# Performance work log

Hardware: AMD Instinct MI355X
Metric: run time of the kernel (lower is better)

The kernel has to match this reference:

```python
import jax, jax.numpy as jnp
import numpy as np

B, T, U, F, H, V = 4, 512, 96, 512, 512, 256
NEG_INF = -1e30


def setup_inputs() -> dict:
    key = jax.random.key(0)
    ks = jax.random.split(key, 7)
    frames = jax.random.normal(ks[0], (B, T, F), dtype=jnp.float32)
    # guarantee num_frames >= num_labels so a valid alignment path exists
    num_frames = jax.random.randint(ks[1], (B,), T // 2, T + 1, dtype=jnp.int32)
    labels = jax.random.randint(ks[2], (B, U), 1, V + 1, dtype=jnp.int32)
    num_labels = jax.random.randint(ks[3], (B,), U // 2, U + 1, dtype=jnp.int32)
    scale = 0.02
    Wf = scale * jax.random.normal(ks[4], (F, H), dtype=jnp.float32)
    E = scale * jax.random.normal(ks[5], (V + 1, H), dtype=jnp.float32)
    Wo = scale * jax.random.normal(ks[6], (H, V + 1), dtype=jnp.float32)
    return dict(frames=frames, num_frames=num_frames, labels=labels,
                num_labels=num_labels, Wf=Wf, E=E, Wo=Wo)


def _lattice_loss(frames, num_frames, labels, num_labels, Wf, E, Wo):
    Bd, Td, _ = frames.shape
    Ud = labels.shape[1]
    # 1-gram context dependency: context state after u emitted labels is
    # 0 (start) if u == 0 else labels[u-1].  ctx: [B, U+1]
    ctx = jnp.concatenate([jnp.zeros((Bd, 1), labels.dtype), labels], axis=1)
    # locally normalized weight fn (RNN-T style joint network)
    fproj = jnp.einsum('btf,fh->bth', frames, Wf)                 # [B,T,H]
    cemb = jnp.take(E, ctx, axis=0)                               # [B,U+1,H]
    h = jnp.tanh(fproj[:, :, None, :] + cemb[:, None, :, :])      # [B,T,U+1,H]
    logits = jax.nn.log_softmax(
        jnp.einsum('btuh,hv->btuv', h, Wo), axis=-1)              # [B,T,U+1,V+1]
    blank = logits[..., 0]                                        # [B,T,U+1]
    # lexical arc weight for emitting label u+1 from state u:
    # lex[b,t,u] = logits[b,t,u, labels[b,u]]
    idx = jnp.broadcast_to(labels[:, None, :, None].astype(jnp.int32),
                           (Bd, Td, Ud, 1))
    lex = jnp.take_along_axis(logits[:, :, :Ud, :], idx, axis=3)[..., 0]  # [B,T,U]

    # forward DP under the Log semiring over the (t, u) string lattice
    alpha0 = jnp.full((Bd, Ud + 1), NEG_INF, dtype=logits.dtype).at[:, 0].set(0.0)

    def step(alpha, xs):
        blank_t, lex_t, t = xs  # [B,U+1], [B,U], scalar
        stay = alpha + blank_t
        emit = jnp.concatenate(
            [jnp.full((Bd, 1), NEG_INF, dtype=alpha.dtype),
             alpha[:, :-1] + lex_t], axis=1)
        new = jnp.logaddexp(stay, emit)
        new = jnp.where((t < num_frames)[:, None], new, alpha)
        return new, None

    xs = (jnp.swapaxes(blank, 0, 1), jnp.swapaxes(lex, 0, 1), jnp.arange(Td))
    alpha, _ = jax.lax.scan(step, alpha0, xs)
    logp = jnp.take_along_axis(alpha, num_labels[:, None].astype(jnp.int32),
                               axis=1)[:, 0]
    return -logp  # [B] negative sequence log-probability


def reference(frames, num_frames, labels, num_labels, Wf, E, Wo):
    return _lattice_loss(frames, num_frames, labels, num_labels, Wf, E, Wo)
```

## Files before the change

kernel.cpp:

```cpp
#include <hip/hip_runtime.h>
#include <hip/hip_bf16.h>


#define BB 4
#define TT 512
#define UU 96
#define FF 512
#define HH 512
#define VV 256
#define NV (VV + 1)
#define NU (UU + 1)
#define NP 272
#define NEG_INF (-1e30f)
#define LOG2E 1.4426950408889634f
#define LN2 0.6931471805599453f
#define NG 128
#define GSTRIDE 520
#define WOSCL 64.0f
#define C2SCL 0.022542110f
#define BCHUNK 17408
#define BLONGS 2176
#define SPLANE 1088

typedef _Float16 f16;
typedef __attribute__((ext_vector_type(2))) _Float16 f16x2;
typedef __attribute__((ext_vector_type(8))) _Float16 f16x8;
typedef __attribute__((ext_vector_type(2))) long longx2;
typedef __bf16 bf16;
typedef __bf16 bf16x8 __attribute__((ext_vector_type(8)));
typedef float f32x4 __attribute__((ext_vector_type(4)));

__device__ __forceinline__ f16x8 splat8(float s) {
    f16 v = (f16)s;
    f16x8 r = {v, v, v, v, v, v, v, v};
    return r;
}

__device__ __forceinline__ long tanh_pack8(f16x8 fv8, f16x8 cv8) {
    f16x8 x = fv8 + cv8;
    x = __builtin_elementwise_min(__builtin_elementwise_max(x, splat8(-2.0f)),
                                  splat8(2.0f));
    f16x8 y = x * x;
    f16x8 q = y * splat8(-0.0067528f) + splat8(0.0700672f);
    q = y * q + splat8(-0.301720f);
    q = y * q + splat8(1.0f);
    f16x8 t = x * q;
    int lo = 0, hi = 0;
    lo = __builtin_amdgcn_cvt_pk_fp8_f32((float)t[0], (float)t[1], lo, false);
    lo = __builtin_amdgcn_cvt_pk_fp8_f32((float)t[2], (float)t[3], lo, true);
    hi = __builtin_amdgcn_cvt_pk_fp8_f32((float)t[4], (float)t[5], hi, false);
    hi = __builtin_amdgcn_cvt_pk_fp8_f32((float)t[6], (float)t[7], hi, true);
    return (long)(((unsigned long long)(unsigned int)lo) |
                  (((unsigned long long)(unsigned int)hi) << 32));
}

__device__ __forceinline__ long pack_fp8x8(const float* v) {
    int lo = 0, hi = 0;
    lo = __builtin_amdgcn_cvt_pk_fp8_f32(v[0], v[1], lo, false);
    lo = __builtin_amdgcn_cvt_pk_fp8_f32(v[2], v[3], lo, true);
    hi = __builtin_amdgcn_cvt_pk_fp8_f32(v[4], v[5], hi, false);
    hi = __builtin_amdgcn_cvt_pk_fp8_f32(v[6], v[7], hi, true);
    return (long)(((unsigned long long)(unsigned int)lo) |
                  (((unsigned long long)(unsigned int)hi) << 32));
}

__device__ __forceinline__ float lae2(float x, float y) {
    float m = fmaxf(x, y);
    float d = fminf(x, y) - m;
    return m + __builtin_amdgcn_logf(1.0f + __builtin_amdgcn_exp2f(d));
}

__device__ __forceinline__ float lse3_2(float x, float y, float z) {
    float m = fmaxf(fmaxf(x, y), z);
    float s = __builtin_amdgcn_exp2f(x - m) + __builtin_amdgcn_exp2f(y - m) +
              __builtin_amdgcn_exp2f(z - m);
    return m + __builtin_amdgcn_logf(s);
}

__device__ __forceinline__ float lse5_2(float a, float b, float c, float d, float e) {
    float m = fmaxf(fmaxf(fmaxf(a, b), fmaxf(c, d)), e);
    float s = __builtin_amdgcn_exp2f(a - m) + __builtin_amdgcn_exp2f(b - m) +
              __builtin_amdgcn_exp2f(c - m) + __builtin_amdgcn_exp2f(d - m) +
              __builtin_amdgcn_exp2f(e - m);
    return m + __builtin_amdgcn_logf(s);
}

__device__ __forceinline__ void async_copy16(const void* g, void* l) {
    __builtin_amdgcn_global_load_lds(
        (const __attribute__((address_space(1))) unsigned int*)g,
        (__attribute__((address_space(3))) unsigned int*)l, 16, 0, 0);
}

__global__ __launch_bounds__(256, 2) void k_front(
    const float* __restrict__ frames, const float* __restrict__ Wf,
    const float* __restrict__ Wo, const float* __restrict__ E,
    const int* __restrict__ labels, f16* __restrict__ fproj,
    long* __restrict__ Wo_s, f16* __restrict__ cemb) {
    __shared__ bf16 Alds[64 * 40];
    __shared__ bf16 Blds[64 * 40];
    const int blk = blockIdx.x;
    const int tid = threadIdx.x;

    if (blk < 256) {
        const int r0 = (blk & 31) * 64;
        const int n0 = (blk >> 5) * 64;
        const int lane = tid & 63, w = tid >> 6;
        const int c = lane & 15, g = lane >> 4;

        const int srow = tid >> 2, sko = (tid & 3) * 8;
        const float* fptr = frames + (size_t)(r0 + srow) * FF + sko;
        const int q = tid >> 6, c64 = tid & 63;

        f32x4 acc[4];
#pragma unroll
        for (int j = 0; j < 4; ++j) acc[j] = (f32x4){0.f, 0.f, 0.f, 0.f};

        for (int kt = 0; kt < FF; kt += 32) {
            float4 f1 = *(const float4*)(fptr + kt);
            float4 f2 = *(const float4*)(fptr + kt + 4);
            bf16x8 av = {(bf16)f1.x, (bf16)f1.y, (bf16)f1.z, (bf16)f1.w,
                         (bf16)f2.x, (bf16)f2.y, (bf16)f2.z, (bf16)f2.w};
            *(bf16x8*)&Alds[srow * 40 + sko] = av;
#pragma unroll
            for (int p = 0; p < 8; ++p) {
                float v = Wf[(size_t)(kt + q * 8 + p) * HH + n0 + c64];
                Blds[c64 * 40 + q * 8 + p] = (bf16)v;
            }
            __syncthreads();
            const int m = w * 16;
            bf16x8 af = *(const bf16x8*)&Alds[(m + c) * 40 + g * 8];
#pragma unroll
            for (int j = 0; j < 4; ++j) {
                bf16x8 bv = *(const bf16x8*)&Blds[(j * 16 + c) * 40 + g * 8];
                acc[j] = __builtin_amdgcn_mfma_f32_16x16x32_bf16(af, bv, acc[j], 0, 0, 0);
            }
            __syncthreads();
        }
        const int m = w * 16;
#pragma unroll
        for (int j = 0; j < 4; ++j)
#pragma unroll
            for (int r = 0; r < 4; ++r)
                fproj[(size_t)(r0 + m + g * 4 + r) * HH + n0 + j * 16 + c] = (f16)acc[j][r];
    } else if (blk < 324) {
        int idx = (blk - 256) * 256 + tid;
        int pos = idx % NP;
        int plane = idx / NP;
        int g = plane & 3;
        int k32 = plane >> 2;
        int n;
        if (pos < 256) {
            int j = ((pos >> 5) << 1) | (pos & 1);
            int cc = (pos >> 1) & 15;
            n = j * 16 + cc;
        } else {
            n = 256 + (pos - 256);
        }
        float v[8];
#pragma unroll
        for (int e = 0; e < 8; ++e) {
            int k = k32 * 32 + g * 8 + e;
            v[e] = (n < NV) ? Wo[k * NV + n] * WOSCL : 0.f;
        }
        Wo_s[idx] = pack_fp8x8(v);
    } else {
        int u = blk - 324;
        for (int b = 0; b < BB; ++b) {
            int ctx = (u == 0) ? 0 : labels[b * UU + (u - 1)];
            const float* src = E + (size_t)ctx * HH;
            f16* dst = cemb + ((size_t)b * NU + u) * HH;
            for (int i = tid; i < HH; i += 256) dst[i] = (f16)src[i];
        }
    }
}

__global__ __launch_bounds__(256, 4) void k_joint(
    const f16* __restrict__ fproj, const f16* __restrict__ cemb,
    const long* __restrict__ Wo_s, const int* __restrict__ labels,
    const int* __restrict__ num_frames, f16* __restrict__ cl_arr) {
    __shared__ __align__(16) long B_s8[2][BLONGS];

    const int tid = threadIdx.x;
    const int b = blockIdx.y;
    const int r0 = blockIdx.x * 64;
    const int nf = num_frames[b];
    if (r0 / NU >= nf) return;

    const int lane = tid & 63, w = tid >> 6;
    const int c = lane & 15, g = lane >> 4;

    const int gr = r0 + w * 16 + c;
    const int at = gr / NU, au = gr - at * NU;
    const f16* pf = fproj + ((size_t)(b * TT + at)) * HH + g * 8;
    const f16* pc = cemb + ((size_t)(b * NU + au)) * HH + g * 8;
    const char* wsrcB = (const char*)Wo_s + lane * 16;

    f32x4 acc[17];
#pragma unroll
    for (int j = 0; j < 17; ++j) acc[j] = (f32x4){0.f, 0.f, 0.f, 0.f};

    const int bB0p = g * NP + (c << 1);
    const int bB16 = g * NP + 256 + c;

    long a0, a1;

    {
        for (int ch = w; ch < 17; ch += 4)
            async_copy16(wsrcB + ch * 1024, (char*)&B_s8[0][0] + ch * 1024 + lane * 16);
        f16x8 fv0 = *(const f16x8*)pf;
        f16x8 cv0 = *(const f16x8*)pc;
        f16x8 fv1 = *(const f16x8*)(pf + 32);
        f16x8 cv1 = *(const f16x8*)(pc + 32);
        a0 = tanh_pack8(fv0, cv0);
        a1 = tanh_pack8(fv1, cv1);
        __syncthreads();
    }

    for (int i = 0; i < 8; ++i) {
        const int cur = i & 1, nxt = cur ^ 1;
        f16x8 fv0, cv0, fv1, cv1;
        if (i < 7) {
            const char* wk = wsrcB + (size_t)(i + 1) * BCHUNK;
            for (int ch = w; ch < 17; ch += 4)
                async_copy16(wk + ch * 1024, (char*)&B_s8[nxt][0] + ch * 1024 + lane * 16);
            const int kt = (i + 1) * 64;
            fv0 = *(const f16x8*)(pf + kt);
            cv0 = *(const f16x8*)(pc + kt);
            fv1 = *(const f16x8*)(pf + kt + 32);
            cv1 = *(const f16x8*)(pc + kt + 32);
        }
        __builtin_amdgcn_s_setprio(1);
#pragma unroll
        for (int p = 0; p < 8; ++p) {
            longx2 bv = *(const longx2*)&B_s8[cur][bB0p + p * 32];
            acc[2 * p] = __builtin_amdgcn_mfma_f32_16x16x32_fp8_fp8(a0, bv[0], acc[2 * p], 0, 0, 0);
            acc[2 * p + 1] = __builtin_amdgcn_mfma_f32_16x16x32_fp8_fp8(a0, bv[1], acc[2 * p + 1], 0, 0, 0);
        }
        acc[16] = __builtin_amdgcn_mfma_f32_16x16x32_fp8_fp8(a0, B_s8[cur][bB16], acc[16], 0, 0, 0);
        __builtin_amdgcn_s_setprio(0);
        long a0n, a1n;
        if (i < 7) {
            a0n = tanh_pack8(fv0, cv0);
            a1n = tanh_pack8(fv1, cv1);
        }
        __builtin_amdgcn_s_setprio(1);
#pragma unroll
        for (int p = 0; p < 8; ++p) {
            longx2 bv = *(const longx2*)&B_s8[cur][SPLANE + bB0p + p * 32];
            acc[2 * p] = __builtin_amdgcn_mfma_f32_16x16x32_fp8_fp8(a1, bv[0], acc[2 * p], 0, 0, 0);
            acc[2 * p + 1] = __builtin_amdgcn_mfma_f32_16x16x32_fp8_fp8(a1, bv[1], acc[2 * p + 1], 0, 0, 0);
        }
        acc[16] = __builtin_amdgcn_mfma_f32_16x16x32_fp8_fp8(a1, B_s8[cur][SPLANE + bB16], acc[16], 0, 0, 0);
        __builtin_amdgcn_s_setprio(0);
        if (i < 7) {
            a0 = a0n;
            a1 = a1n;
            __syncthreads();
        }
    }

    const int rbase = r0 + w * 16 + g * 4;
    f16x8 ovs;
#pragma unroll
    for (int r = 0; r < 4; ++r) {
        const int grr = rbase + r;
        const int u = grr - (grr / NU) * NU;

        float mx = NEG_INF;
#pragma unroll
        for (int j = 0; j < 17; ++j) {
            int col = j * 16 + c;
            if (col < NV) mx = fmaxf(mx, acc[j][r]);
        }
#pragma unroll
        for (int s = 1; s < 16; s <<= 1) mx = fmaxf(mx, __shfl_xor(mx, s));
        float mxc = mx * C2SCL;
        float sum = 0.f;
#pragma unroll
        for (int j = 0; j < 17; ++j) {
            int col = j * 16 + c;
            if (col < NV)
                sum += __builtin_amdgcn_exp2f(fmaf(acc[j][r], C2SCL, -mxc));
        }
#pragma unroll
        for (int s = 1; s < 16; s <<= 1) sum += __shfl_xor(sum, s);
        float lse2 = mxc + __builtin_amdgcn_logf(sum);

        float blankv = __shfl(acc[0][r], lane & 48);
        int L = (u < UU) ? labels[b * UU + u] : 0;
        int jl = L >> 4;
        float v = acc[0][r];
#pragma unroll
        for (int j = 1; j < 17; ++j)
            if (jl == j) v = acc[j][r];
        float lexv = __shfl(v, (lane & 48) | (L & 15));

        ovs[2 * r] = (f16)fmaf(blankv, C2SCL, -lse2);
        ovs[2 * r + 1] = (u < UU) ? (f16)fmaf(lexv, C2SCL, -lse2) : (f16)0.f;
    }
    if (c == 0)
        *(f16x8*)&cl_arr[((size_t)b * TT * NU + rbase) * 2] = ovs;
}

__global__ __launch_bounds__(128) void k_compact(
    const f16* __restrict__ cl, const int* __restrict__ num_frames,
    float* __restrict__ Dg) {
    const int g = blockIdx.x;
    const int b = blockIdx.y;
    const int u = threadIdx.x;
    if (u >= NU) return;
    const int nf = num_frames[b];
    const f16x2* P = (const f16x2*)(cl + (size_t)b * TT * NU * 2);

    auto fetch = [&](int t, int uu, float& bb, float& ll) {
        if (uu <= UU) {
            f16x2 z = P[t * NU + uu];
            bool act = t < nf;
            bb = act ? (float)z.x : 0.f;
            ll = (act && uu < UU) ? (float)z.y : NEG_INF;
        } else {
            bb = NEG_INF;
            ll = NEG_INF;
        }
    };

    const int t0 = g * 4;
    float b0, l0, b1u, l1u, b1u1, l1u1;
    fetch(t0, u, b0, l0);
    fetch(t0 + 1, u, b1u, l1u);
    fetch(t0 + 1, u + 1, b1u1, l1u1);
    float A0 = b0 + b1u;
    float A1 = lae2(l0 + b1u1, b0 + l1u);
    float A2 = l0 + l1u1;
    float B0[3], B1[3], B2[3];
#pragma unroll
    for (int j = 0; j < 3; ++j) {
        float b2v, l2v, b3v, l3v, b3n, l3n;
        fetch(t0 + 2, u + j, b2v, l2v);
        fetch(t0 + 3, u + j, b3v, l3v);
        fetch(t0 + 3, u + j + 1, b3n, l3n);
        B0[j] = b2v + b3v;
        B1[j] = lae2(l2v + b3n, b2v + l3v);
        B2[j] = l2v + l3n;
    }
    float* d = Dg + ((size_t)b * NG + g) * GSTRIDE;
    d[u] = A0 + B0[0];
    d[104 + u] = lae2(A1 + B0[1], A0 + B1[0]);
    d[208 + u] = lse3_2(A2 + B0[2], A1 + B1[1], A0 + B2[0]);
    d[312 + u] = lae2(A2 + B1[2], A1 + B2[1]);
    d[416 + u] = A2 + B2[2];
}

__global__ __launch_bounds__(64) void k_dpser(
    const float* __restrict__ Dg, const int* __restrict__ num_labels,
    float* __restrict__ out) {
    const int b = blockIdx.x;
    const int lane = threadIdx.x;
    const float* D = Dg + (size_t)b * NG * GSTRIDE;
    const int lo_u = lane;
    const int hi_u = 64 + ((lane < 33) ? lane : 0);

    float a_lo = (lane == 0) ? 0.f : NEG_INF;
    float a_hi = NEG_INF;

    constexpr int R = 8;
    float blo[R][5], bhi[R][5];
#pragma unroll
    for (int g = 0; g < R; ++g)
#pragma unroll
        for (int k = 0; k < 5; ++k) {
            blo[g][k] = D[g * GSTRIDE + k * 104 + lo_u];
            bhi[g][k] = D[g * GSTRIDE + k * 104 + hi_u];
        }

#pragma unroll 8
    for (int g = 0; g < NG; ++g) {
        const int slot = g & (R - 1);
        float el[5], eh[5];
#pragma unroll
        for (int k = 0; k < 5; ++k) {
            el[k] = a_lo + blo[slot][k];
            eh[k] = a_hi + bhi[slot][k];
        }
        const int gp = g + R;
        if (gp < NG) {
#pragma unroll
            for (int k = 0; k < 5; ++k) {
                blo[slot][k] = D[gp * GSTRIDE + k * 104 + lo_u];
                bhi[slot][k] = D[gp * GSTRIDE + k * 104 + hi_u];
            }
        }
        float ml[5], mh[5];
        ml[0] = el[0];
        mh[0] = eh[0];
#pragma unroll
        for (int k = 1; k < 5; ++k) {
            float su = __shfl_up(el[k], k);
            ml[k] = (lane >= k) ? su : NEG_INF;
            float sh = __shfl_up(eh[k], k);
            float xl = __shfl(el[k], 64 - k + lane);
            mh[k] = (lane >= k) ? sh : xl;
        }
        a_lo = lse5_2(ml[0], ml[1], ml[2], ml[3], ml[4]);
        float nh = lse5_2(mh[0], mh[1], mh[2], mh[3], mh[4]);
        if (lane < 33) a_hi = nh;
    }

    const int nl = num_labels[b];
    float res = (nl < 64) ? __shfl(a_lo, nl) : __shfl(a_hi, nl - 64);
    if (lane == 0) out[b] = -res * LN2;
}

extern "C" void kernel_launch(void* const* d_in, const int* in_sizes, int n_in,
                              void* d_out, int out_size, void* d_ws, size_t ws_size,
                              hipStream_t stream) {
    const float* frames = (const float*)d_in[0];
    const int* num_frames = (const int*)d_in[1];
    const int* labels = (const int*)d_in[2];
    const int* num_labels = (const int*)d_in[3];
    const float* Wf = (const float*)d_in[4];
    const float* E = (const float*)d_in[5];
    const float* Wo = (const float*)d_in[6];
    float* out = (float*)d_out;

    char* ws = (char*)d_ws;
    size_t off = 0;
    long* Wo_s = (long*)(ws + off); off += (size_t)17408 * 8;
    f16* cemb = (f16*)(ws + off); off += (size_t)BB * NU * HH * 2;
    off = (off + 255) & ~(size_t)255;
    f16* fproj = (f16*)(ws + off); off += (size_t)BB * TT * HH * 2;
    off = (off + 255) & ~(size_t)255;
    f16* cl_arr = (f16*)(ws + off); off += (size_t)BB * TT * NU * 2 * 2;
    off = (off + 255) & ~(size_t)255;
    float* Dg = (float*)(ws + off); off += (size_t)BB * NG * GSTRIDE * 4;

    hipLaunchKernelGGL(k_front, dim3(421), dim3(256), 0, stream,
                       frames, Wf, Wo, E, labels, fproj, Wo_s, cemb);
    hipLaunchKernelGGL(k_joint, dim3((TT * NU) / 64, BB), dim3(256), 0, stream,
                       fproj, cemb, Wo_s, labels, num_frames, cl_arr);
    hipLaunchKernelGGL(k_compact, dim3(NG, BB), dim3(128), 0, stream,
                       cl_arr, num_frames, Dg);
    hipLaunchKernelGGL(k_dpser, dim3(BB), dim3(64), 0, stream,
                       Dg, num_labels, out);
}
```

Baseline: 182.3 us.

## Stage serial DP band data through LDS with async triple-buffered copies

The serial DP kernel now streams each batch's precomputed band coefficients into a three-chunk LDS ring buffer using async 16-byte global-to-LDS copies, and reads the per-group values from LDS instead of global memory. The register prefetch depth drops from 8 to 4 groups, and GSTRIDE grows to 640 so each chunk is a whole number of 1 KB copy blocks. The goal is to hide global load latency on this single-wavefront serial recurrence. It relies on hand-written vmcnt waits whose counts must match the number of issued copies, and it adds padding to the intermediate buffer.

```diff
diff --git a/kernel.cpp b/kernel.cpp
--- a/kernel.cpp
+++ b/kernel.cpp
@@ -15,12 +15,16 @@
 #define LOG2E 1.4426950408889634f
 #define LN2 0.6931471805599453f
 #define NG 128
-#define GSTRIDE 520
+#define GSTRIDE 640
 #define WOSCL 64.0f
 #define C2SCL 0.022542110f
 #define BCHUNK 17408
 #define BLONGS 2176
 #define SPLANE 1088
+#define CHG 8
+#define CHB (CHG * GSTRIDE * 4)
+#define CHI (CHB / 1024)
+#define CHF (CHG * GSTRIDE)
 
 typedef _Float16 f16;
 typedef __attribute__((ext_vector_type(2))) _Float16 f16x2;
@@ -354,56 +358,83 @@
 __global__ __launch_bounds__(64) void k_dpser(
     const float* __restrict__ Dg, const int* __restrict__ num_labels,
     float* __restrict__ out) {
+    __shared__ __align__(16) float Dl[3 * CHF];
     const int b = blockIdx.x;
     const int lane = threadIdx.x;
-    const float* D = Dg + (size_t)b * NG * GSTRIDE;
+    const char* Db = (const char*)(Dg + (size_t)b * NG * GSTRIDE);
     const int lo_u = lane;
     const int hi_u = 64 + ((lane < 33) ? lane : 0);
 
+    auto stage = [&](int q) {
+        const char* src = Db + (size_t)q * CHB + lane * 16;
+        char* dst = (char*)Dl + (q % 3) * CHB + lane * 16;
+#pragma unroll
+        for (int i = 0; i < CHI; ++i)
+            async_copy16(src + i * 1024, dst + i * 1024);
+    };
+
+    stage(0);
+    stage(1);
+    asm volatile("s_waitcnt vmcnt(20)" ::: "memory");
+
     float a_lo = (lane == 0) ? 0.f : NEG_INF;
     float a_hi = NEG_INF;
 
-    constexpr int R = 8;
+    constexpr int R = 4;
     float blo[R][5], bhi[R][5];
 #pragma unroll
     for (int g = 0; g < R; ++g)
 #pragma unroll
         for (int k = 0; k < 5; ++k) {
-            blo[g][k] = D[g * GSTRIDE + k * 104 + lo_u];
-            bhi[g][k] = D[g * GSTRIDE + k * 104 + hi_u];
-        }
-
-#pragma unroll 8
-    for (int g = 0; g < NG; ++g) {
-        const int slot = g & (R - 1);
-        float el[5], eh[5];
-#pragma unroll
-        for (int k = 0; k < 5; ++k) {
-            el[k] = a_lo + blo[slot][k];
-            eh[k] = a_hi + bhi[slot][k];
-        }
-        const int gp = g + R;
-        if (gp < NG) {
+            blo[g][k] = Dl[g * GSTRIDE + k * 104 + lo_u];
+            bhi[g][k] = Dl[g * GSTRIDE + k * 104 + hi_u];
+        }
+
+    int bc = 0;
+    int bn = CHF;
+    for (int c = 0; c < NG / CHG; ++c) {
+        if (c + 2 < NG / CHG) {
+            stage(c + 2);
+            asm volatile("s_waitcnt vmcnt(20)" ::: "memory");
+        } else {
+            asm volatile("s_waitcnt vmcnt(0)" ::: "memory");
+        }
+#pragma unroll
+        for (int g8 = 0; g8 < CHG; ++g8) {
+            const int slot = g8 & 3;
+            float el[5], eh[5];
 #pragma unroll
             for (int k = 0; k < 5; ++k) {
-                blo[slot][k] = D[gp * GSTRIDE + k * 104 + lo_u];
-                bhi[slot][k] = D[gp * GSTRIDE + k * 104 + hi_u];
+                el[k] = a_lo + blo[slot][k];
+                eh[k] = a_hi + bhi[slot][k];
             }
-        }
-        float ml[5], mh[5];
-        ml[0] = el[0];
-        mh[0] = eh[0];
-#pragma unroll
-        for (int k = 1; k < 5; ++k) {
-            float su = __shfl_up(el[k], k);
-            ml[k] = (lane >= k) ? su : NEG_INF;
-            float sh = __shfl_up(eh[k], k);
-            float xl = __shfl(el[k], 64 - k + lane);
-            mh[k] = (lane >= k) ? sh : xl;
-        }
-        a_lo = lse5_2(ml[0], ml[1], ml[2], ml[3], ml[4]);
-        float nh = lse5_2(mh[0], mh[1], mh[2], mh[3], mh[4]);
-        if (lane < 33) a_hi = nh;
+            const int g = c * CHG + g8;
+            if (g + 4 < NG) {
+                const int rb = (g8 < 4) ? bc : bn;
+                const int rs = (g8 + 4) & 7;
+#pragma unroll
+                for (int k = 0; k < 5; ++k) {
+                    blo[slot][k] = Dl[rb + rs * GSTRIDE + k * 104 + lo_u];
+                    bhi[slot][k] = Dl[rb + rs * GSTRIDE + k * 104 + hi_u];
+                }
+            }
+            float ml[5], mh[5];
+            ml[0] = el[0];
+            mh[0] = eh[0];
+#pragma unroll
+            for (int k = 1; k < 5; ++k) {
+                float su = __shfl_up(el[k], k);
+                ml[k] = (lane >= k) ? su : NEG_INF;
+                float sh = __shfl_up(eh[k], k);
+                float xl = __shfl(el[k], 64 - k + lane);
+                mh[k] = (lane >= k) ? sh : xl;
+            }
+            a_lo = lse5_2(ml[0], ml[1], ml[2], ml[3], ml[4]);
+            float nh = lse5_2(mh[0], mh[1], mh[2], mh[3], mh[4]);
+            if (lane < 33) a_hi = nh;
+        }
+        bc = bn;
+        bn = (bn == 2 * CHF) ? 0 : bn + CHF;
     }
 
     const int nl = num_labels[b];
```

Result: faster. 168.0 us (-7.8%).

## Compose 8-step lattice transfers to halve serial DP steps, stage via LDS

Applied to the files above, without the earlier changes.

The compact kernel now builds each frame group's transfer band from 8 timesteps instead of 4. It does this by combining two depth-4 bands through shared memory into a 9-diagonal log-semiring band. The serial DP kernel therefore runs 64 dependent steps instead of 128, at the cost of 9-term log-sum-exp and more shuffles per step. The band data is also prefetched into LDS in chunks with async global-to-LDS copies and vmcnt waits, replacing direct global register prefetch. The goal is to shorten the latency-bound single-wavefront recurrence, in exchange for extra parallel work in the compact stage.

```diff
diff --git a/kernel.cpp b/kernel.cpp
--- a/kernel.cpp
+++ b/kernel.cpp
@@ -9,18 +9,22 @@
 #define HH 512
 #define VV 256
 #define NV (VV + 1)
-#define NU (UU + 1)
+#define NU 97
 #define NP 272
 #define NEG_INF (-1e30f)
-#define LOG2E 1.4426950408889634f
 #define LN2 0.6931471805599453f
-#define NG 128
-#define GSTRIDE 520
 #define WOSCL 64.0f
 #define C2SCL 0.022542110f
 #define BCHUNK 17408
 #define BLONGS 2176
 #define SPLANE 1088
+#define NG2 64
+#define GS2 960
+#define CH2G 4
+#define CH2B (CH2G * GS2 * 4)
+#define CH2I (CH2B / 1024)
+#define CH2F (CH2G * GS2)
+#define NCH 16
 
 typedef _Float16 f16;
 typedef __attribute__((ext_vector_type(2))) _Float16 f16x2;
@@ -85,6 +89,17 @@
     return m + __builtin_amdgcn_logf(s);
 }
 
+__device__ __forceinline__ float lse9_2(const float* v) {
+    float m1 = fmaxf(fmaxf(v[0], v[1]), v[2]);
+    float m2 = fmaxf(fmaxf(v[3], v[4]), v[5]);
+    float m3 = fmaxf(fmaxf(v[6], v[7]), v[8]);
+    float m = fmaxf(fmaxf(m1, m2), m3);
+    float s = 0.f;
+#pragma unroll
+    for (int k = 0; k < 9; ++k) s += __builtin_amdgcn_exp2f(v[k] - m);
+    return m + __builtin_amdgcn_logf(s);
+}
+
 __device__ __forceinline__ void async_copy16(const void* g, void* l) {
     __builtin_amdgcn_global_load_lds(
         (const __attribute__((address_space(1))) unsigned int*)g,
@@ -305,10 +320,10 @@
 __global__ __launch_bounds__(128) void k_compact(
     const f16* __restrict__ cl, const int* __restrict__ num_frames,
     float* __restrict__ Dg) {
+    __shared__ float Bl[5][128];
     const int g = blockIdx.x;
     const int b = blockIdx.y;
     const int u = threadIdx.x;
-    if (u >= NU) return;
     const int nf = num_frames[b];
     const f16x2* P = (const f16x2*)(cl + (size_t)b * TT * NU * 2);
 
@@ -324,86 +339,146 @@
         }
     };
 
-    const int t0 = g * 4;
-    float b0, l0, b1u, l1u, b1u1, l1u1;
-    fetch(t0, u, b0, l0);
-    fetch(t0 + 1, u, b1u, l1u);
-    fetch(t0 + 1, u + 1, b1u1, l1u1);
-    float A0 = b0 + b1u;
-    float A1 = lae2(l0 + b1u1, b0 + l1u);
-    float A2 = l0 + l1u1;
-    float B0[3], B1[3], B2[3];
-#pragma unroll
-    for (int j = 0; j < 3; ++j) {
-        float b2v, l2v, b3v, l3v, b3n, l3n;
-        fetch(t0 + 2, u + j, b2v, l2v);
-        fetch(t0 + 3, u + j, b3v, l3v);
-        fetch(t0 + 3, u + j + 1, b3n, l3n);
-        B0[j] = b2v + b3v;
-        B1[j] = lae2(l2v + b3n, b2v + l3v);
-        B2[j] = l2v + l3n;
+    auto depth4 = [&](int t0, float* D) {
+        float b0, l0, b1u, l1u, b1u1, l1u1;
+        fetch(t0, u, b0, l0);
+        fetch(t0 + 1, u, b1u, l1u);
+        fetch(t0 + 1, u + 1, b1u1, l1u1);
+        float A0 = b0 + b1u;
+        float A1 = lae2(l0 + b1u1, b0 + l1u);
+        float A2 = l0 + l1u1;
+        float B0[3], B1[3], B2[3];
+#pragma unroll
+        for (int j = 0; j < 3; ++j) {
+            float b2v, l2v, b3v, l3v, b3n, l3n;
+            fetch(t0 + 2, u + j, b2v, l2v);
+            fetch(t0 + 3, u + j, b3v, l3v);
+            fetch(t0 + 3, u + j + 1, b3n, l3n);
+            B0[j] = b2v + b3v;
+            B1[j] = lae2(l2v + b3n, b2v + l3v);
+            B2[j] = l2v + l3n;
+        }
+        D[0] = A0 + B0[0];
+        D[1] = lae2(A1 + B0[1], A0 + B1[0]);
+        D[2] = lse3_2(A2 + B0[2], A1 + B1[1], A0 + B2[0]);
+        D[3] = lae2(A2 + B1[2], A1 + B2[1]);
+        D[4] = A2 + B2[2];
+    };
+
+    float Da[5], Db[5];
+    depth4(g * 8, Da);
+    depth4(g * 8 + 4, Db);
+#pragma unroll
+    for (int k = 0; k < 5; ++k) Bl[k][u] = Db[k];
+    __syncthreads();
+
+    if (u < 104) {
+        float d0 = Da[0] + Bl[0][u];
+        float d1 = lae2(Da[0] + Bl[1][u], Da[1] + Bl[0][u + 1]);
+        float d2 = lse3_2(Da[0] + Bl[2][u], Da[1] + Bl[1][u + 1],
+                          Da[2] + Bl[0][u + 2]);
+        float d3 = lae2(lae2(Da[0] + Bl[3][u], Da[1] + Bl[2][u + 1]),
+                        lae2(Da[2] + Bl[1][u + 2], Da[3] + Bl[0][u + 3]));
+        float d4 = lse5_2(Da[0] + Bl[4][u], Da[1] + Bl[3][u + 1],
+                          Da[2] + Bl[2][u + 2], Da[3] + Bl[1][u + 3],
+                          Da[4] + Bl[0][u + 4]);
+        float d5 = lae2(lae2(Da[1] + Bl[4][u + 1], Da[2] + Bl[3][u + 2]),
+                        lae2(Da[3] + Bl[2][u + 3], Da[4] + Bl[1][u + 4]));
+        float d6 = lse3_2(Da[2] + Bl[4][u + 2], Da[3] + Bl[3][u + 3],
+                          Da[4] + Bl[2][u + 4]);
+        float d7 = lae2(Da[3] + Bl[4][u + 3], Da[4] + Bl[3][u + 4]);
+        float d8 = Da[4] + Bl[4][u + 4];
+        float* d = Dg + ((size_t)b * NG2 + g) * GS2;
+        d[u] = d0;
+        d[104 + u] = d1;
+        d[208 + u] = d2;
+        d[312 + u] = d3;
+        d[416 + u] = d4;
+        d[520 + u] = d5;
+        d[624 + u] = d6;
+        d[728 + u] = d7;
+        d[832 + u] = d8;
     }
-    float* d = Dg + ((size_t)b * NG + g) * GSTRIDE;
-    d[u] = A0 + B0[0];
-    d[104 + u] = lae2(A1 + B0[1], A0 + B1[0]);
-    d[208 + u] = lse3_2(A2 + B0[2], A1 + B1[1], A0 + B2[0]);
-    d[312 + u] = lae2(A2 + B1[2], A1 + B2[1]);
-    d[416 + u] = A2 + B2[2];
 }
 
 __global__ __launch_bounds__(64) void k_dpser(
     const float* __restrict__ Dg, const int* __restrict__ num_labels,
     float* __restrict__ out) {
+    __shared__ __align__(16) float Dl[4 * CH2F];
     const int b = blockIdx.x;
     const int lane = threadIdx.x;
-    const float* D = Dg + (size_t)b * NG * GSTRIDE;
+    const char* Db = (const char*)(Dg + (size_t)b * NG2 * GS2);
     const int lo_u = lane;
     const int hi_u = 64 + ((lane < 33) ? lane : 0);
 
+    auto stage = [&](int q) {
+        const char* src = Db + (size_t)q * CH2B + lane * 16;
+        char* dst = (char*)Dl + (q & 3) * CH2B + lane * 16;
+#pragma unroll
+        for (int i = 0; i < CH2I; ++i)
+            async_copy16(src + i * 1024, dst + i * 1024);
+    };
+
+    stage(0);
+    stage(1);
+    stage(2);
+    asm volatile("s_waitcnt vmcnt(30)" ::: "memory");
+
     float a_lo = (lane == 0) ? 0.f : NEG_INF;
     float a_hi = NEG_INF;
 
-    constexpr int R = 8;
-    float blo[R][5], bhi[R][5];
-#pragma unroll
-    for (int g = 0; g < R; ++g)
-#pragma unroll
-        for (int k = 0; k < 5; ++k) {
-            blo[g][k] = D[g * GSTRIDE + k * 104 + lo_u];
-            bhi[g][k] = D[g * GSTRIDE + k * 104 + hi_u];
-        }
-
-#pragma unroll 8
-    for (int g = 0; g < NG; ++g) {
-        const int slot = g & (R - 1);
-        float el[5], eh[5];
-#pragma unroll
-        for (int k = 0; k < 5; ++k) {
-            el[k] = a_lo + blo[slot][k];
-            eh[k] = a_hi + bhi[slot][k];
-        }
-        const int gp = g + R;
-        if (gp < NG) {
-#pragma unroll
-            for (int k = 0; k < 5; ++k) {
-                blo[slot][k] = D[gp * GSTRIDE + k * 104 + lo_u];
-                bhi[slot][k] = D[gp * GSTRIDE + k * 104 + hi_u];
+    float blo[4][9], bhi[4][9];
+#pragma unroll
+    for (int g = 0; g < 4; ++g)
+#pragma unroll
+        for (int k = 0; k < 9; ++k) {
+            blo[g][k] = Dl[g * GS2 + k * 104 + lo_u];
+            bhi[g][k] = Dl[g * GS2 + k * 104 + hi_u];
+        }
+
+    for (int c = 0; c < NCH; ++c) {
+        if (c + 3 < NCH) {
+            stage(c + 3);
+            asm volatile("s_waitcnt vmcnt(30)" ::: "memory");
+        } else if (c + 2 < NCH) {
+            asm volatile("s_waitcnt vmcnt(15)" ::: "memory");
+        } else {
+            asm volatile("s_waitcnt vmcnt(0)" ::: "memory");
+        }
+#pragma unroll
+        for (int g8 = 0; g8 < CH2G; ++g8) {
+            const int slot = g8;
+            float el[9], eh[9];
+#pragma unroll
+            for (int k = 0; k < 9; ++k) {
+                el[k] = a_lo + blo[slot][k];
+                eh[k] = a_hi + bhi[slot][k];
             }
-        }
-        float ml[5], mh[5];
-        ml[0] = el[0];
-        mh[0] = eh[0];
-#pragma unroll
-        for (int k = 1; k < 5; ++k) {
-            float su = __shfl_up(el[k], k);
-            ml[k] = (lane >= k) ? su : NEG_INF;
-            float sh = __shfl_up(eh[k], k);
-            float xl = __shfl(el[k], 64 - k + lane);
-            mh[k] = (lane >= k) ? sh : xl;
-        }
-        a_lo = lse5_2(ml[0], ml[1], ml[2], ml[3], ml[4]);
-        float nh = lse5_2(mh[0], mh[1], mh[2], mh[3], mh[4]);
-        if (lane < 33) a_hi = nh;
+            const int g = c * CH2G + g8;
+            if (g + 4 < NG2) {
+                const int q = g + 4;
+                const int base = ((q >> 2) & 3) * CH2F + (q & 3) * GS2;
+#pragma unroll
+                for (int k = 0; k < 9; ++k) {
+                    blo[slot][k] = Dl[base + k * 104 + lo_u];
+                    bhi[slot][k] = Dl[base + k * 104 + hi_u];
+                }
+            }
+            float ml[9], mh[9];
+            ml[0] = el[0];
+            mh[0] = eh[0];
+#pragma unroll
+            for (int k = 1; k < 9; ++k) {
+                float su = __shfl_up(el[k], k);
+                ml[k] = (lane >= k) ? su : NEG_INF;
+                float sh = __shfl_up(eh[k], k);
+                float xl = __shfl(el[k], 64 - k + lane);
+                mh[k] = (lane >= k) ? sh : xl;
+            }
+            a_lo = lse9_2(ml);
+            float nh = lse9_2(mh);
+            if (lane < 33) a_hi = nh;
+        }
     }
 
     const int nl = num_labels[b];
@@ -432,13 +507,13 @@
     off = (off + 255) & ~(size_t)255;
     f16* cl_arr = (f16*)(ws + off); off += (size_t)BB * TT * NU * 2 * 2;
     off = (off + 255) & ~(size_t)255;
-    float* Dg = (float*)(ws + off); off += (size_t)BB * NG * GSTRIDE * 4;
+    float* Dg = (float*)(ws + off); off += (size_t)BB * NG2 * GS2 * 4;
 
     hipLaunchKernelGGL(k_front, dim3(421), dim3(256), 0, stream,
                        frames, Wf, Wo, E, labels, fproj, Wo_s, cemb);
     hipLaunchKernelGGL(k_joint, dim3((TT * NU) / 64, BB), dim3(256), 0, stream,
                        fproj, cemb, Wo_s, labels, num_frames, cl_arr);
-    hipLaunchKernelGGL(k_compact, dim3(NG, BB), dim3(128), 0, stream,
+    hipLaunchKernelGGL(k_compact, dim3(NG2, BB), dim3(128), 0, stream,
                        cl_arr, num_frames, Dg);
     hipLaunchKernelGGL(k_dpser, dim3(BB), dim3(64), 0, stream,
                        Dg, num_labels, out);
```

Result: faster. 168.6 us (-7.5%).
